# Optimization experiments

Measured on AMD Instinct MI355X. Metric: run time of the kernel, lower is better.

Reference implementation:

```python
import jax, jax.numpy as jnp
import numpy as np
import math

E_IN, E_OUT = 512, 96
B, QL, PL = 64, 128, 196

def _lin(k, shape):
    fan_in = shape[1]
    bound = 1.0 / math.sqrt(fan_in)
    k1, k2 = jax.random.split(k)
    W = jax.random.uniform(k1, shape, jnp.float32, -bound, bound)
    b = jax.random.uniform(k2, (shape[0],), jnp.float32, -bound, bound)
    return W, b

def setup_inputs() -> dict:
    key = jax.random.key(0)
    ks = jax.random.split(key, 16)
    inp = {
        'z_d_cls': jax.random.normal(ks[0], (B, E_IN), jnp.float32),
        'Z_d_tok': jax.random.normal(ks[1], (B, QL, E_IN), jnp.float32),
        'z_t_cls': jax.random.normal(ks[2], (B, E_IN), jnp.float32),
        'Z_t_tok': jax.random.normal(ks[3], (B, QL, E_IN), jnp.float32),
        'z_v_cls': jax.random.normal(ks[4], (B, E_IN), jnp.float32),
        'Z_v_patch': jax.random.normal(ks[5], (B, PL, E_IN), jnp.float32),
    }
    names = ['t_cls', 'd_cls', 'v_cls', 't_tok', 'v_patch', 'tgl_q', 'tgl_k', 'tgl_v']
    for i, n in enumerate(names):
        W, b = _lin(ks[6 + i], (E_OUT, E_IN))
        inp[f'W_{n}'] = W
        inp[f'b_{n}'] = b
    inp['ln_g'] = jnp.ones((E_OUT,), jnp.float32)
    inp['ln_b'] = jnp.zeros((E_OUT,), jnp.float32)
    return inp

def _l2n(x, eps=1e-6):
    return x / jnp.maximum(jnp.linalg.norm(x, axis=-1, keepdims=True), eps)

def _proj(x, W, b):
    return x @ W.T + b

def _layer_norm(x, g, b, eps=1e-5):
    mu = jnp.mean(x, axis=-1, keepdims=True)
    var = jnp.mean((x - mu) ** 2, axis=-1, keepdims=True)
    return (x - mu) / jnp.sqrt(var + eps) * g + b

def reference(z_d_cls, Z_d_tok, z_t_cls, Z_t_tok, z_v_cls, Z_v_patch,
              W_t_cls, b_t_cls, W_d_cls, b_d_cls, W_v_cls, b_v_cls,
              W_t_tok, b_t_tok, W_v_patch, b_v_patch,
              W_tgl_q, b_tgl_q, W_tgl_k, b_tgl_k, W_tgl_v, b_tgl_v,
              ln_g, ln_b):
    # --- TGG: global-global text/doc cosine sim [B, B]
    t = _l2n(_proj(z_t_cls, W_t_cls, b_t_cls))
    d = _l2n(_proj(z_d_cls, W_d_cls, b_d_cls))
    S_TGG = t @ d.T
    # --- TGL: cross-attention over all batch pairs
    Q = _proj(Z_d_tok, W_tgl_q, b_tgl_q)   # [b, q, h]
    K = _proj(Z_t_tok, W_tgl_k, b_tgl_k)   # [c, k, h]
    V = _proj(Z_t_tok, W_tgl_v, b_tgl_v)   # [c, k, h]
    scores = jnp.einsum('bqh,ckh->bcqk', Q, K) / math.sqrt(E_OUT)
    attn = jax.nn.softmax(scores, axis=-1)
    context = jnp.einsum('bcqk,ckh->bcqh', attn, V).mean(axis=2)  # [b, c, h]
    context = _layer_norm(context, ln_g, ln_b)
    S_TGL = jnp.einsum('ih,ijh->ij', d, _l2n(context))
    S_TIB = 0.5 * (S_TGG + S_TGL)
    # --- CGG: global-global text/vision cosine sim
    v = _l2n(_proj(z_v_cls, W_v_cls, b_v_cls))
    S_CGG = t @ v.T
    # --- CLL: token-patch max similarity
    t_tok = _l2n(_proj(Z_t_tok, W_t_tok, b_t_tok))        # [b, t, h]
    v_pat = _l2n(_proj(Z_v_patch, W_v_patch, b_v_patch))  # [c, p, h]
    sim = jnp.einsum('bth,cph->bctp', t_tok, v_pat)
    S_CLL = sim.max(axis=(-1, -2))
    S_CAB = 0.5 * (S_CGG + S_CLL)
    return S_TIB + S_CAB
```

## Files before the change

### kernel.cpp

```cpp
#include <hip/hip_runtime.h>
#include <hip/hip_bf16.h>
#include <math.h>

typedef __bf16 bf16;
typedef __attribute__((ext_vector_type(8))) __bf16 bf16x8;
typedef __attribute__((ext_vector_type(2))) float f32x2;
typedef __attribute__((ext_vector_type(4))) float f32x4;
typedef __attribute__((ext_vector_type(4))) unsigned int uint4v;

#define MFMA16(a, b, c) __builtin_amdgcn_mfma_f32_16x16x32_bf16(a, b, c, 0, 0, 0)

#define QSCALE 0.14724450f

__device__ __forceinline__ bf16x8 cvt8v(f32x4 lo, f32x4 hi) {
    bf16x8 r;
    r[0] = (bf16)lo[0]; r[1] = (bf16)lo[1]; r[2] = (bf16)lo[2]; r[3] = (bf16)lo[3];
    r[4] = (bf16)hi[0]; r[5] = (bf16)hi[1]; r[6] = (bf16)hi[2]; r[7] = (bf16)hi[3];
    return r;
}


struct WPtrs { const float* W[8]; };

__global__ __launch_bounds__(256) void cvtw_kernel(WPtrs wp, bf16* __restrict__ Wb) {
    int j   = blockIdx.x / 48;
    int blk = blockIdx.x - j * 48;
    int idx = (blk * 256 + threadIdx.x) * 4;
    f32x4 v = *(const f32x4*)(wp.W[j] + idx);
    bf16* dst = Wb + j * 49152 + idx;
    dst[0] = (bf16)v[0]; dst[1] = (bf16)v[1]; dst[2] = (bf16)v[2]; dst[3] = (bf16)v[3];
}


struct ProjParams {
    const float* src[8];
    const float* B[8];
    void* dst[8];
    const bf16* Wb;
};

__global__ __launch_bounds__(256) void proj_kernel(ProjParams p) {
    int w = threadIdx.x >> 6, lane = threadIdx.x & 63;
    int gw = blockIdx.x * 4 + w;
    int m = lane & 15, quad = lane >> 4;

    int job, t0;
    if      (gw < 256)  { job = 3; t0 = gw; }
    else if (gw < 512)  { job = 4; t0 = gw - 256; }
    else if (gw < 768)  { job = 5; t0 = gw - 512; }
    else if (gw < 1024) { job = 6; t0 = gw - 768; }
    else if (gw < 1416) { job = 7; t0 = gw - 1024; }
    else if (gw < 1422) { int r = gw - 1416; job = r >> 1; t0 = r & 1; }
    else return;
    int r0 = t0 << 5;

    const float* X = p.src[job] + (size_t)(r0 + m) * 512 + quad * 8;
    const bf16*  W = p.Wb + job * 49152 + (size_t)m * 512 + quad * 8;

    f32x4 acc[2][6] = {};
    #pragma unroll
    for (int kk = 0; kk < 512; kk += 32) {
        bf16x8 a0 = cvt8v(*(const f32x4*)(X + kk),
                          *(const f32x4*)(X + kk + 4));
        bf16x8 a1 = cvt8v(*(const f32x4*)(X + 16 * 512 + kk),
                          *(const f32x4*)(X + 16 * 512 + kk + 4));
        #pragma unroll
        for (int nt = 0; nt < 6; nt++) {
            bf16x8 b = *(const bf16x8*)(W + (size_t)nt * 16 * 512 + kk);
            acc[0][nt] = MFMA16(a0, b, acc[0][nt]);
            acc[1][nt] = MFMA16(a1, b, acc[1][nt]);
        }
    }

    bool  norm  = (job < 3) || (job >= 6);
    float scale = (job == 3) ? QSCALE : 1.0f;
    const float* Bv = p.B[job];
    float bb[6];
    #pragma unroll
    for (int nt = 0; nt < 6; nt++) bb[nt] = Bv[nt * 16 + m];

    #pragma unroll
    for (int rt = 0; rt < 2; rt++)
        #pragma unroll
        for (int nt = 0; nt < 6; nt++)
            #pragma unroll
            for (int r = 0; r < 4; r++)
                acc[rt][nt][r] = (acc[rt][nt][r] + bb[nt]) * scale;

    if (norm) {
        #pragma unroll
        for (int rt = 0; rt < 2; rt++)
            #pragma unroll
            for (int r = 0; r < 4; r++) {
                float s = 0.0f;
                #pragma unroll
                for (int nt = 0; nt < 6; nt++) s += acc[rt][nt][r] * acc[rt][nt][r];
                s += __shfl_xor(s, 1); s += __shfl_xor(s, 2);
                s += __shfl_xor(s, 4); s += __shfl_xor(s, 8);
                float inv = 1.0f / fmaxf(sqrtf(s), 1e-6f);
                #pragma unroll
                for (int nt = 0; nt < 6; nt++) acc[rt][nt][r] *= inv;
            }
    }

    if (job < 3) {
        float* dst = (float*)p.dst[job];
        #pragma unroll
        for (int rt = 0; rt < 2; rt++)
            #pragma unroll
            for (int r = 0; r < 4; r++)
                #pragma unroll
                for (int nt = 0; nt < 6; nt++)
                    dst[(size_t)(r0 + rt * 16 + quad * 4 + r) * 96 + nt * 16 + m] = acc[rt][nt][r];
    } else {
        bf16* dst = (bf16*)p.dst[job];
        #pragma unroll
        for (int rt = 0; rt < 2; rt++)
            #pragma unroll
            for (int r = 0; r < 4; r++)
                #pragma unroll
                for (int nt = 0; nt < 6; nt++)
                    dst[(size_t)(r0 + rt * 16 + quad * 4 + r) * 96 + nt * 16 + m] = (bf16)acc[rt][nt][r];
    }
}


__global__ __launch_bounds__(256) void attn_kernel(
    const bf16* __restrict__ Qg, const bf16* __restrict__ Kg, const bf16* __restrict__ Vg,
    float* __restrict__ Ctx)
{
    int pr = blockIdx.x;
    int b = pr >> 6, c = pr & 63;
    int tid = threadIdx.x, lane = tid & 63, w = tid >> 6;
    int m = lane & 15, quad = lane >> 4;
    const bf16* Q = Qg + (size_t)b * (128 * 96);
    const bf16* K = Kg + (size_t)c * (128 * 96);
    const bf16* V = Vg + (size_t)c * (128 * 96);

    __shared__ __align__(16) bf16 Klds[128 * 104];
    #pragma unroll
    for (int it = 0; it < 6; it++) {
        int ch = it * 256 + tid;
        int row = ch / 12, seg = ch - row * 12;
        *(uint4v*)(Klds + row * 104 + seg * 8) = *(const uint4v*)(K + ch * 8);
    }
    __syncthreads();

    f32x4 acc[2][8] = {};
    #pragma unroll
    for (int kk = 0; kk < 96; kk += 32) {
        bf16x8 a0 = *(const bf16x8*)(Q + (size_t)(w * 32 + m) * 96 + kk + quad * 8);
        bf16x8 a1 = *(const bf16x8*)(Q + (size_t)(w * 32 + 16 + m) * 96 + kk + quad * 8);
        #pragma unroll
        for (int nt = 0; nt < 8; nt++) {
            bf16x8 bb = *(const bf16x8*)(Klds + (nt * 16 + m) * 104 + kk + quad * 8);
            acc[0][nt] = MFMA16(a0, bb, acc[0][nt]);
            acc[1][nt] = MFMA16(a1, bb, acc[1][nt]);
        }
    }
    float wpart[8];
    #pragma unroll
    for (int nt = 0; nt < 8; nt++) wpart[nt] = 0.0f;
    #pragma unroll
    for (int mt = 0; mt < 2; mt++) {
        #pragma unroll
        for (int r = 0; r < 4; r++) {
            float tv[8]; float s = 0.0f;
            #pragma unroll
            for (int nt = 0; nt < 8; nt++) { tv[nt] = exp2f(acc[mt][nt][r]); s += tv[nt]; }
            s += __shfl_xor(s, 1); s += __shfl_xor(s, 2);
            s += __shfl_xor(s, 4); s += __shfl_xor(s, 8);
            float inv = 1.0f / s;
            #pragma unroll
            for (int nt = 0; nt < 8; nt++) wpart[nt] += tv[nt] * inv;
        }
    }
    #pragma unroll
    for (int nt = 0; nt < 8; nt++) {
        wpart[nt] += __shfl_xor(wpart[nt], 16);
        wpart[nt] += __shfl_xor(wpart[nt], 32);
    }
    __shared__ float wsum4[4][128];
    __shared__ float wk[128];
    __shared__ float ctxp[4][96];
    if (lane < 16) {
        #pragma unroll
        for (int nt = 0; nt < 8; nt++) wsum4[w][nt * 16 + lane] = wpart[nt];
    }
    __syncthreads();
    if (tid < 128) wk[tid] = wsum4[0][tid] + wsum4[1][tid] + wsum4[2][tid] + wsum4[3][tid];
    __syncthreads();
    {
        float c0 = 0.0f, c1 = 0.0f;
        if (lane < 48) {
            #pragma unroll 4
            for (int r = 0; r < 32; r++) {
                int k = w * 32 + r;
                unsigned u = *(const unsigned*)(V + (size_t)k * 96 + lane * 2);
                float lo = __uint_as_float(u << 16);
                float hi = __uint_as_float(u & 0xffff0000u);
                float wkk = wk[k];
                c0 += wkk * lo; c1 += wkk * hi;
            }
            ctxp[w][lane * 2]     = c0;
            ctxp[w][lane * 2 + 1] = c1;
        }
    }
    __syncthreads();
    if (tid < 96)
        Ctx[(size_t)pr * 96 + tid] =
            (ctxp[0][tid] + ctxp[1][tid] + ctxp[2][tid] + ctxp[3][tid]) * (1.0f / 128.0f);
}


__global__ __launch_bounds__(256) void cll_kernel(
    const bf16* __restrict__ Tt, const bf16* __restrict__ Vp,
    const float* __restrict__ Ctx, const float* __restrict__ t,
    const float* __restrict__ d, const float* __restrict__ v,
    const float* __restrict__ ln_g, const float* __restrict__ ln_b,
    float* __restrict__ out)
{
    int c = blockIdx.x >> 3, bg = blockIdx.x & 7;
    int tid = threadIdx.x, lane = tid & 63, w = tid >> 6;
    int m = lane & 15, quad = lane >> 4;
    const bf16* P = Vp + (size_t)c * (196 * 96);

    __shared__ __align__(16) bf16 Plds[196 * 104];
    __shared__ float red[8][4];
    for (int ch = tid; ch < 2352; ch += 256) {
        int row = ch / 12, seg = ch - row * 12;
        *(uint4v*)(Plds + row * 104 + seg * 8) = *(const uint4v*)(P + ch * 8);
    }
    int rofs[13];
    #pragma unroll
    for (int nt = 0; nt < 13; nt++) {
        int r = nt * 16 + m; if (r > 195) r = 195;
        rofs[nt] = r * 104;
    }
    __syncthreads();

    for (int bi = 0; bi < 8; bi++) {
        const bf16* T = Tt + (size_t)(bg * 8 + bi) * (128 * 96);
        f32x4 acc[2][13] = {};
        #pragma unroll
        for (int kk = 0; kk < 96; kk += 32) {
            bf16x8 a0 = *(const bf16x8*)(T + (size_t)(w * 32 + m) * 96 + kk + quad * 8);
            bf16x8 a1 = *(const bf16x8*)(T + (size_t)(w * 32 + 16 + m) * 96 + kk + quad * 8);
            #pragma unroll
            for (int nt = 0; nt < 13; nt++) {
                bf16x8 bb = *(const bf16x8*)(Plds + rofs[nt] + kk + quad * 8);
                acc[0][nt] = MFMA16(a0, bb, acc[0][nt]);
                acc[1][nt] = MFMA16(a1, bb, acc[1][nt]);
            }
        }
        float mx = -3.4e38f;
        #pragma unroll
        for (int mt = 0; mt < 2; mt++)
            #pragma unroll
            for (int nt = 0; nt < 13; nt++)
                #pragma unroll
                for (int r = 0; r < 4; r++) mx = fmaxf(mx, acc[mt][nt][r]);
        #pragma unroll
        for (int dd = 1; dd < 64; dd <<= 1) mx = fmaxf(mx, __shfl_xor(mx, dd));
        if (lane == 0) red[bi][w] = mx;
    }
    __syncthreads();

    #pragma unroll
    for (int half = 0; half < 2; half++) {
        int bi = w + half * 4;
        int i  = bg * 8 + bi;
        int pr = i * 64 + c;
        float scll = fmaxf(fmaxf(red[bi][0], red[bi][1]), fmaxf(red[bi][2], red[bi][3]));
        bool act = lane < 48;
        float c0 = 0, c1 = 0, t0 = 0, t1 = 0;
        float dj0 = 0, dj1 = 0, di0 = 0, di1 = 0, v0 = 0, v1 = 0, g0 = 0, g1 = 0, bb0 = 0, bb1 = 0;
        if (act) {
            f32x2 cc  = *(const f32x2*)(Ctx + (size_t)pr * 96 + lane * 2);
            f32x2 tt  = *(const f32x2*)(t + i * 96 + lane * 2);
            f32x2 ddj = *(const f32x2*)(d + c * 96 + lane * 2);
            f32x2 ddi = *(const f32x2*)(d + i * 96 + lane * 2);
            f32x2 vv  = *(const f32x2*)(v + c * 96 + lane * 2);
            f32x2 gg  = *(const f32x2*)(ln_g + lane * 2);
            f32x2 bbv = *(const f32x2*)(ln_b + lane * 2);
            c0 = cc[0]; c1 = cc[1]; t0 = tt[0]; t1 = tt[1];
            dj0 = ddj[0]; dj1 = ddj[1]; di0 = ddi[0]; di1 = ddi[1];
            v0 = vv[0]; v1 = vv[1];
            g0 = gg[0]; g1 = gg[1]; bb0 = bbv[0]; bb1 = bbv[1];
        }
        float s = c0 + c1;
        #pragma unroll
        for (int k = 1; k < 64; k <<= 1) s += __shfl_xor(s, k);
        float mean = s * (1.0f / 96.0f);
        float e0 = act ? (c0 - mean) : 0.0f;
        float e1 = act ? (c1 - mean) : 0.0f;
        float q = e0 * e0 + e1 * e1;
        #pragma unroll
        for (int k = 1; k < 64; k <<= 1) q += __shfl_xor(q, k);
        float rstd = rsqrtf(q * (1.0f / 96.0f) + 1e-5f);
        float y0 = act ? (e0 * rstd * g0 + bb0) : 0.0f;
        float y1 = act ? (e1 * rstd * g1 + bb1) : 0.0f;
        float dot = y0 * di0 + y1 * di1;
        float ssq = y0 * y0 + y1 * y1;
        float tg  = t0 * dj0 + t1 * dj1;
        float cg  = t0 * v0 + t1 * v1;
        #pragma unroll
        for (int k = 1; k < 64; k <<= 1) {
            dot += __shfl_xor(dot, k); ssq += __shfl_xor(ssq, k);
            tg  += __shfl_xor(tg, k);  cg  += __shfl_xor(cg, k);
        }
        if (lane == 0) {
            float stgl = dot / fmaxf(sqrtf(ssq), 1e-6f);
            out[pr] = 0.5f * (tg + stgl) + 0.5f * (cg + scll);
        }
    }
}


extern "C" void kernel_launch(void* const* d_in, const int* in_sizes, int n_in,
                              void* d_out, int out_size, void* d_ws, size_t ws_size,
                              hipStream_t stream)
{
    (void)in_sizes; (void)n_in; (void)out_size; (void)ws_size;
    char* ws = (char*)d_ws;
    float* t     = (float*)(ws + 0);
    float* d     = (float*)(ws + 24576);
    float* v     = (float*)(ws + 49152);
    bf16* Wb = (bf16*)(ws + 106496);
    bf16* Qb = (bf16*)(ws + 892928);
    bf16* Kb = (bf16*)(ws + 892928 + 1572864);
    bf16* Vb = (bf16*)(ws + 892928 + 2 * 1572864);
    bf16* Tt = (bf16*)(ws + 892928 + 3 * 1572864);
    bf16* Vp = (bf16*)(ws + 892928 + 4 * 1572864);
    float* Ctx = (float*)(ws + 892928 + 4 * 1572864 + 2408448);

    WPtrs wp;
    wp.W[0] = (const float*)d_in[6];
    wp.W[1] = (const float*)d_in[8];
    wp.W[2] = (const float*)d_in[10];
    wp.W[3] = (const float*)d_in[16];
    wp.W[4] = (const float*)d_in[18];
    wp.W[5] = (const float*)d_in[20];
    wp.W[6] = (const float*)d_in[12];
    wp.W[7] = (const float*)d_in[14];
    hipLaunchKernelGGL(cvtw_kernel, dim3(384), dim3(256), 0, stream, wp, Wb);

    ProjParams pp;
    pp.Wb = Wb;
    pp.src[0] = (const float*)d_in[2];  pp.B[0] = (const float*)d_in[7];  pp.dst[0] = t;
    pp.src[1] = (const float*)d_in[0];  pp.B[1] = (const float*)d_in[9];  pp.dst[1] = d;
    pp.src[2] = (const float*)d_in[4];  pp.B[2] = (const float*)d_in[11]; pp.dst[2] = v;
    pp.src[3] = (const float*)d_in[1];  pp.B[3] = (const float*)d_in[17]; pp.dst[3] = Qb;
    pp.src[4] = (const float*)d_in[3];  pp.B[4] = (const float*)d_in[19]; pp.dst[4] = Kb;
    pp.src[5] = (const float*)d_in[3];  pp.B[5] = (const float*)d_in[21]; pp.dst[5] = Vb;
    pp.src[6] = (const float*)d_in[3];  pp.B[6] = (const float*)d_in[13]; pp.dst[6] = Tt;
    pp.src[7] = (const float*)d_in[5];  pp.B[7] = (const float*)d_in[15]; pp.dst[7] = Vp;
    hipLaunchKernelGGL(proj_kernel, dim3(356), dim3(256), 0, stream, pp);

    hipLaunchKernelGGL(attn_kernel, dim3(4096), dim3(256), 0, stream,
                       (const bf16*)Qb, (const bf16*)Kb, (const bf16*)Vb, Ctx);
    hipLaunchKernelGGL(cll_kernel, dim3(512), dim3(256), 0, stream,
                       (const bf16*)Tt, (const bf16*)Vp,
                       (const float*)Ctx, (const float*)t, (const float*)d, (const float*)v,
                       (const float*)d_in[22], (const float*)d_in[23], (float*)d_out);
}
```

Before: 240.7 us.

## Drop weight-conversion kernel, XOR-swizzle LDS tiles, prefetch V into registers

```diff
diff --git a/kernel.cpp b/kernel.cpp
--- a/kernel.cpp
+++ b/kernel.cpp
@@ -20,23 +20,11 @@
 }
 
 
-struct WPtrs { const float* W[8]; };
-
-__global__ __launch_bounds__(256) void cvtw_kernel(WPtrs wp, bf16* __restrict__ Wb) {
-    int j   = blockIdx.x / 48;
-    int blk = blockIdx.x - j * 48;
-    int idx = (blk * 256 + threadIdx.x) * 4;
-    f32x4 v = *(const f32x4*)(wp.W[j] + idx);
-    bf16* dst = Wb + j * 49152 + idx;
-    dst[0] = (bf16)v[0]; dst[1] = (bf16)v[1]; dst[2] = (bf16)v[2]; dst[3] = (bf16)v[3];
-}
-
-
 struct ProjParams {
     const float* src[8];
+    const float* W[8];
     const float* B[8];
     void* dst[8];
-    const bf16* Wb;
 };
 
 __global__ __launch_bounds__(256) void proj_kernel(ProjParams p) {
@@ -54,8 +42,8 @@
     else return;
     int r0 = t0 << 5;
 
-    const float* X = p.src[job] + (size_t)(r0 + m) * 512 + quad * 8;
-    const bf16*  W = p.Wb + job * 49152 + (size_t)m * 512 + quad * 8;
+    const float* X  = p.src[job] + (size_t)(r0 + m) * 512 + quad * 8;
+    const float* Wf = p.W[job] + (size_t)m * 512 + quad * 8;
 
     f32x4 acc[2][6] = {};
     #pragma unroll
@@ -66,7 +54,8 @@
                           *(const f32x4*)(X + 16 * 512 + kk + 4));
         #pragma unroll
         for (int nt = 0; nt < 6; nt++) {
-            bf16x8 b = *(const bf16x8*)(W + (size_t)nt * 16 * 512 + kk);
+            const float* wp = Wf + (size_t)nt * 16 * 512 + kk;
+            bf16x8 b = cvt8v(*(const f32x4*)wp, *(const f32x4*)(wp + 4));
             acc[0][nt] = MFMA16(a0, b, acc[0][nt]);
             acc[1][nt] = MFMA16(a1, b, acc[1][nt]);
         }
@@ -137,15 +126,18 @@
     const bf16* K = Kg + (size_t)c * (128 * 96);
     const bf16* V = Vg + (size_t)c * (128 * 96);
 
-    __shared__ __align__(16) bf16 Klds[128 * 104];
+    __shared__ __align__(16) bf16 Klds[128 * 96];
+    char* kb = (char*)Klds;
     #pragma unroll
     for (int it = 0; it < 6; it++) {
         int ch = it * 256 + tid;
         int row = ch / 12, seg = ch - row * 12;
-        *(uint4v*)(Klds + row * 104 + seg * 8) = *(const uint4v*)(K + ch * 8);
-    }
-    __syncthreads();
-
+        int addr = (row * 192 + seg * 16) ^ ((row & 7) << 4);
+        *(uint4v*)(kb + addr) = *(const uint4v*)(K + ch * 8);
+    }
+    __syncthreads();
+
+    int kx = (m & 7) << 4;
     f32x4 acc[2][8] = {};
     #pragma unroll
     for (int kk = 0; kk < 96; kk += 32) {
@@ -153,11 +145,20 @@
         bf16x8 a1 = *(const bf16x8*)(Q + (size_t)(w * 32 + 16 + m) * 96 + kk + quad * 8);
         #pragma unroll
         for (int nt = 0; nt < 8; nt++) {
-            bf16x8 bb = *(const bf16x8*)(Klds + (nt * 16 + m) * 104 + kk + quad * 8);
+            int addr = ((nt * 16 + m) * 192 + kk * 2 + quad * 16) ^ kx;
+            bf16x8 bb = *(const bf16x8*)(kb + addr);
             acc[0][nt] = MFMA16(a0, bb, acc[0][nt]);
             acc[1][nt] = MFMA16(a1, bb, acc[1][nt]);
         }
     }
+
+    unsigned vr[32];
+    if (lane < 48) {
+        #pragma unroll
+        for (int r = 0; r < 32; r++)
+            vr[r] = *(const unsigned*)(V + (size_t)(w * 32 + r) * 96 + lane * 2);
+    }
+
     float wpart[8];
     #pragma unroll
     for (int nt = 0; nt < 8; nt++) wpart[nt] = 0.0f;
@@ -170,7 +171,7 @@
             for (int nt = 0; nt < 8; nt++) { tv[nt] = exp2f(acc[mt][nt][r]); s += tv[nt]; }
             s += __shfl_xor(s, 1); s += __shfl_xor(s, 2);
             s += __shfl_xor(s, 4); s += __shfl_xor(s, 8);
-            float inv = 1.0f / s;
+            float inv = __builtin_amdgcn_rcpf(s);
             #pragma unroll
             for (int nt = 0; nt < 8; nt++) wpart[nt] += tv[nt] * inv;
         }
@@ -193,14 +194,12 @@
     {
         float c0 = 0.0f, c1 = 0.0f;
         if (lane < 48) {
-            #pragma unroll 4
+            #pragma unroll
             for (int r = 0; r < 32; r++) {
-                int k = w * 32 + r;
-                unsigned u = *(const unsigned*)(V + (size_t)k * 96 + lane * 2);
-                float lo = __uint_as_float(u << 16);
-                float hi = __uint_as_float(u & 0xffff0000u);
-                float wkk = wk[k];
-                c0 += wkk * lo; c1 += wkk * hi;
+                unsigned u = vr[r];
+                float wkk = wk[w * 32 + r];
+                c0 += wkk * __uint_as_float(u << 16);
+                c1 += wkk * __uint_as_float(u & 0xffff0000u);
             }
             ctxp[w][lane * 2]     = c0;
             ctxp[w][lane * 2 + 1] = c1;
@@ -225,17 +224,20 @@
     int m = lane & 15, quad = lane >> 4;
     const bf16* P = Vp + (size_t)c * (196 * 96);
 
-    __shared__ __align__(16) bf16 Plds[196 * 104];
+    __shared__ __align__(16) bf16 Plds[196 * 96];
     __shared__ float red[8][4];
+    char* pb = (char*)Plds;
     for (int ch = tid; ch < 2352; ch += 256) {
         int row = ch / 12, seg = ch - row * 12;
-        *(uint4v*)(Plds + row * 104 + seg * 8) = *(const uint4v*)(P + ch * 8);
-    }
-    int rofs[13];
+        int addr = (row * 192 + seg * 16) ^ ((row & 7) << 4);
+        *(uint4v*)(pb + addr) = *(const uint4v*)(P + ch * 8);
+    }
+    int rofs[13], rx[13];
     #pragma unroll
     for (int nt = 0; nt < 13; nt++) {
         int r = nt * 16 + m; if (r > 195) r = 195;
-        rofs[nt] = r * 104;
+        rofs[nt] = r * 192 + quad * 16;
+        rx[nt]   = (r & 7) << 4;
     }
     __syncthreads();
 
@@ -248,7 +250,7 @@
             bf16x8 a1 = *(const bf16x8*)(T + (size_t)(w * 32 + 16 + m) * 96 + kk + quad * 8);
             #pragma unroll
             for (int nt = 0; nt < 13; nt++) {
-                bf16x8 bb = *(const bf16x8*)(Plds + rofs[nt] + kk + quad * 8);
+                bf16x8 bb = *(const bf16x8*)(pb + ((rofs[nt] + kk * 2) ^ rx[nt]));
                 acc[0][nt] = MFMA16(a0, bb, acc[0][nt]);
                 acc[1][nt] = MFMA16(a1, bb, acc[1][nt]);
             }
@@ -326,7 +328,6 @@
     float* t     = (float*)(ws + 0);
     float* d     = (float*)(ws + 24576);
     float* v     = (float*)(ws + 49152);
-    bf16* Wb = (bf16*)(ws + 106496);
     bf16* Qb = (bf16*)(ws + 892928);
     bf16* Kb = (bf16*)(ws + 892928 + 1572864);
     bf16* Vb = (bf16*)(ws + 892928 + 2 * 1572864);
@@ -334,27 +335,15 @@
     bf16* Vp = (bf16*)(ws + 892928 + 4 * 1572864);
     float* Ctx = (float*)(ws + 892928 + 4 * 1572864 + 2408448);
 
-    WPtrs wp;
-    wp.W[0] = (const float*)d_in[6];
-    wp.W[1] = (const float*)d_in[8];
-    wp.W[2] = (const float*)d_in[10];
-    wp.W[3] = (const float*)d_in[16];
-    wp.W[4] = (const float*)d_in[18];
-    wp.W[5] = (const float*)d_in[20];
-    wp.W[6] = (const float*)d_in[12];
-    wp.W[7] = (const float*)d_in[14];
-    hipLaunchKernelGGL(cvtw_kernel, dim3(384), dim3(256), 0, stream, wp, Wb);
-
     ProjParams pp;
-    pp.Wb = Wb;
-    pp.src[0] = (const float*)d_in[2];  pp.B[0] = (const float*)d_in[7];  pp.dst[0] = t;
-    pp.src[1] = (const float*)d_in[0];  pp.B[1] = (const float*)d_in[9];  pp.dst[1] = d;
-    pp.src[2] = (const float*)d_in[4];  pp.B[2] = (const float*)d_in[11]; pp.dst[2] = v;
-    pp.src[3] = (const float*)d_in[1];  pp.B[3] = (const float*)d_in[17]; pp.dst[3] = Qb;
-    pp.src[4] = (const float*)d_in[3];  pp.B[4] = (const float*)d_in[19]; pp.dst[4] = Kb;
-    pp.src[5] = (const float*)d_in[3];  pp.B[5] = (const float*)d_in[21]; pp.dst[5] = Vb;
-    pp.src[6] = (const float*)d_in[3];  pp.B[6] = (const float*)d_in[13]; pp.dst[6] = Tt;
-    pp.src[7] = (const float*)d_in[5];  pp.B[7] = (const float*)d_in[15]; pp.dst[7] = Vp;
+    pp.src[0] = (const float*)d_in[2];  pp.W[0] = (const float*)d_in[6];  pp.B[0] = (const float*)d_in[7];  pp.dst[0] = t;
+    pp.src[1] = (const float*)d_in[0];  pp.W[1] = (const float*)d_in[8];  pp.B[1] = (const float*)d_in[9];  pp.dst[1] = d;
+    pp.src[2] = (const float*)d_in[4];  pp.W[2] = (const float*)d_in[10]; pp.B[2] = (const float*)d_in[11]; pp.dst[2] = v;
+    pp.src[3] = (const float*)d_in[1];  pp.W[3] = (const float*)d_in[16]; pp.B[3] = (const float*)d_in[17]; pp.dst[3] = Qb;
+    pp.src[4] = (const float*)d_in[3];  pp.W[4] = (const float*)d_in[18]; pp.B[4] = (const float*)d_in[19]; pp.dst[4] = Kb;
+    pp.src[5] = (const float*)d_in[3];  pp.W[5] = (const float*)d_in[20]; pp.B[5] = (const float*)d_in[21]; pp.dst[5] = Vb;
+    pp.src[6] = (const float*)d_in[3];  pp.W[6] = (const float*)d_in[12]; pp.B[6] = (const float*)d_in[13]; pp.dst[6] = Tt;
+    pp.src[7] = (const float*)d_in[5];  pp.W[7] = (const float*)d_in[14]; pp.B[7] = (const float*)d_in[15]; pp.dst[7] = Vp;
     hipLaunchKernelGGL(proj_kernel, dim3(356), dim3(256), 0, stream, pp);
 
     hipLaunchKernelGGL(attn_kernel, dim3(4096), dim3(256), 0, stream,
```

Measured after the change: 264.5 us. 9.9% more time.

## Fuse K/V/T projections sharing input, swizzle LDS, prefetch V in attention

Applied to the files above, without the earlier changes.

```diff
diff --git a/kernel.cpp b/kernel.cpp
--- a/kernel.cpp
+++ b/kernel.cpp
@@ -44,83 +44,112 @@
     int gw = blockIdx.x * 4 + w;
     int m = lane & 15, quad = lane >> 4;
 
-    int job, t0;
-    if      (gw < 256)  { job = 3; t0 = gw; }
-    else if (gw < 512)  { job = 4; t0 = gw - 256; }
-    else if (gw < 768)  { job = 5; t0 = gw - 512; }
-    else if (gw < 1024) { job = 6; t0 = gw - 768; }
-    else if (gw < 1416) { job = 7; t0 = gw - 1024; }
-    else if (gw < 1422) { int r = gw - 1416; job = r >> 1; t0 = r & 1; }
-    else return;
-    int r0 = t0 << 5;
-
-    const float* X = p.src[job] + (size_t)(r0 + m) * 512 + quad * 8;
-    const bf16*  W = p.Wb + job * 49152 + (size_t)m * 512 + quad * 8;
-
-    f32x4 acc[2][6] = {};
-    #pragma unroll
-    for (int kk = 0; kk < 512; kk += 32) {
-        bf16x8 a0 = cvt8v(*(const f32x4*)(X + kk),
-                          *(const f32x4*)(X + kk + 4));
-        bf16x8 a1 = cvt8v(*(const f32x4*)(X + 16 * 512 + kk),
-                          *(const f32x4*)(X + 16 * 512 + kk + 4));
-        #pragma unroll
-        for (int nt = 0; nt < 6; nt++) {
-            bf16x8 b = *(const bf16x8*)(W + (size_t)nt * 16 * 512 + kk);
-            acc[0][nt] = MFMA16(a0, b, acc[0][nt]);
-            acc[1][nt] = MFMA16(a1, b, acc[1][nt]);
-        }
-    }
-
-    bool  norm  = (job < 3) || (job >= 6);
-    float scale = (job == 3) ? QSCALE : 1.0f;
-    const float* Bv = p.B[job];
-    float bb[6];
-    #pragma unroll
-    for (int nt = 0; nt < 6; nt++) bb[nt] = Bv[nt * 16 + m];
-
-    #pragma unroll
-    for (int rt = 0; rt < 2; rt++)
-        #pragma unroll
-        for (int nt = 0; nt < 6; nt++)
-            #pragma unroll
-            for (int r = 0; r < 4; r++)
-                acc[rt][nt][r] = (acc[rt][nt][r] + bb[nt]) * scale;
-
-    if (norm) {
-        #pragma unroll
-        for (int rt = 0; rt < 2; rt++)
-            #pragma unroll
-            for (int r = 0; r < 4; r++) {
-                float s = 0.0f;
+    if (gw >= 512 && gw < 1024) {
+        int r0 = (gw - 512) << 4;
+        const float* X  = p.src[4] + (size_t)(r0 + m) * 512 + quad * 8;
+        const bf16*  W4 = p.Wb + 4 * 49152 + (size_t)m * 512 + quad * 8;
+
+        f32x4 acc[3][6] = {};
+        #pragma unroll
+        for (int kk = 0; kk < 512; kk += 32) {
+            bf16x8 a = cvt8v(*(const f32x4*)(X + kk), *(const f32x4*)(X + kk + 4));
+            #pragma unroll
+            for (int j = 0; j < 3; j++)
                 #pragma unroll
-                for (int nt = 0; nt < 6; nt++) s += acc[rt][nt][r] * acc[rt][nt][r];
-                s += __shfl_xor(s, 1); s += __shfl_xor(s, 2);
-                s += __shfl_xor(s, 4); s += __shfl_xor(s, 8);
-                float inv = 1.0f / fmaxf(sqrtf(s), 1e-6f);
+                for (int nt = 0; nt < 6; nt++) {
+                    bf16x8 b = *(const bf16x8*)(W4 + j * 49152 + (size_t)nt * 16 * 512 + kk);
+                    acc[j][nt] = MFMA16(a, b, acc[j][nt]);
+                }
+        }
+        #pragma unroll
+        for (int j = 0; j < 3; j++) {
+            const float* Bv = p.B[4 + j];
+            #pragma unroll
+            for (int nt = 0; nt < 6; nt++) {
+                float bv = Bv[nt * 16 + m];
                 #pragma unroll
-                for (int nt = 0; nt < 6; nt++) acc[rt][nt][r] *= inv;
+                for (int r = 0; r < 4; r++) acc[j][nt][r] += bv;
             }
-    }
-
-    if (job < 3) {
-        float* dst = (float*)p.dst[job];
-        #pragma unroll
-        for (int rt = 0; rt < 2; rt++)
+            if (j == 2) {
+                #pragma unroll
+                for (int r = 0; r < 4; r++) {
+                    float s = 0.0f;
+                    #pragma unroll
+                    for (int nt = 0; nt < 6; nt++) s += acc[2][nt][r] * acc[2][nt][r];
+                    s += __shfl_xor(s, 1); s += __shfl_xor(s, 2);
+                    s += __shfl_xor(s, 4); s += __shfl_xor(s, 8);
+                    float inv = 1.0f / fmaxf(sqrtf(s), 1e-6f);
+                    #pragma unroll
+                    for (int nt = 0; nt < 6; nt++) acc[2][nt][r] *= inv;
+                }
+            }
+            bf16* dst = (bf16*)p.dst[4 + j];
             #pragma unroll
             for (int r = 0; r < 4; r++)
                 #pragma unroll
                 for (int nt = 0; nt < 6; nt++)
-                    dst[(size_t)(r0 + rt * 16 + quad * 4 + r) * 96 + nt * 16 + m] = acc[rt][nt][r];
+                    dst[(size_t)(r0 + quad * 4 + r) * 96 + nt * 16 + m] = (bf16)acc[j][nt][r];
+        }
+        return;
+    }
+
+    int job, t0;
+    if      (gw < 512)  { job = 3; t0 = gw; }
+    else if (gw < 1808) { job = 7; t0 = gw - 1024; }
+    else if (gw < 1820) { int r = gw - 1808; job = r >> 2; t0 = r & 3; }
+    else return;
+    int r0 = t0 << 4;
+
+    const float* X = p.src[job] + (size_t)(r0 + m) * 512 + quad * 8;
+    const bf16*  W = p.Wb + job * 49152 + (size_t)m * 512 + quad * 8;
+
+    f32x4 acc[6] = {};
+    #pragma unroll
+    for (int kk = 0; kk < 512; kk += 32) {
+        bf16x8 a = cvt8v(*(const f32x4*)(X + kk), *(const f32x4*)(X + kk + 4));
+        #pragma unroll
+        for (int nt = 0; nt < 6; nt++) {
+            bf16x8 b = *(const bf16x8*)(W + (size_t)nt * 16 * 512 + kk);
+            acc[nt] = MFMA16(a, b, acc[nt]);
+        }
+    }
+
+    bool  norm  = (job != 3);
+    float scale = (job == 3) ? QSCALE : 1.0f;
+    const float* Bv = p.B[job];
+    #pragma unroll
+    for (int nt = 0; nt < 6; nt++) {
+        float bv = Bv[nt * 16 + m];
+        #pragma unroll
+        for (int r = 0; r < 4; r++) acc[nt][r] = (acc[nt][r] + bv) * scale;
+    }
+    if (norm) {
+        #pragma unroll
+        for (int r = 0; r < 4; r++) {
+            float s = 0.0f;
+            #pragma unroll
+            for (int nt = 0; nt < 6; nt++) s += acc[nt][r] * acc[nt][r];
+            s += __shfl_xor(s, 1); s += __shfl_xor(s, 2);
+            s += __shfl_xor(s, 4); s += __shfl_xor(s, 8);
+            float inv = 1.0f / fmaxf(sqrtf(s), 1e-6f);
+            #pragma unroll
+            for (int nt = 0; nt < 6; nt++) acc[nt][r] *= inv;
+        }
+    }
+    if (job < 3) {
+        float* dst = (float*)p.dst[job];
+        #pragma unroll
+        for (int r = 0; r < 4; r++)
+            #pragma unroll
+            for (int nt = 0; nt < 6; nt++)
+                dst[(size_t)(r0 + quad * 4 + r) * 96 + nt * 16 + m] = acc[nt][r];
     } else {
         bf16* dst = (bf16*)p.dst[job];
         #pragma unroll
-        for (int rt = 0; rt < 2; rt++)
-            #pragma unroll
-            for (int r = 0; r < 4; r++)
-                #pragma unroll
-                for (int nt = 0; nt < 6; nt++)
-                    dst[(size_t)(r0 + rt * 16 + quad * 4 + r) * 96 + nt * 16 + m] = (bf16)acc[rt][nt][r];
+        for (int r = 0; r < 4; r++)
+            #pragma unroll
+            for (int nt = 0; nt < 6; nt++)
+                dst[(size_t)(r0 + quad * 4 + r) * 96 + nt * 16 + m] = (bf16)acc[nt][r];
     }
 }
 
@@ -137,15 +166,18 @@
     const bf16* K = Kg + (size_t)c * (128 * 96);
     const bf16* V = Vg + (size_t)c * (128 * 96);
 
-    __shared__ __align__(16) bf16 Klds[128 * 104];
+    __shared__ __align__(16) bf16 Klds[128 * 96];
+    char* kb = (char*)Klds;
     #pragma unroll
     for (int it = 0; it < 6; it++) {
         int ch = it * 256 + tid;
         int row = ch / 12, seg = ch - row * 12;
-        *(uint4v*)(Klds + row * 104 + seg * 8) = *(const uint4v*)(K + ch * 8);
-    }
-    __syncthreads();
-
+        int addr = (row * 192 + seg * 16) ^ ((row & 7) << 4);
+        *(uint4v*)(kb + addr) = *(const uint4v*)(K + ch * 8);
+    }
+    __syncthreads();
+
+    int kx = (m & 7) << 4;
     f32x4 acc[2][8] = {};
     #pragma unroll
     for (int kk = 0; kk < 96; kk += 32) {
@@ -153,11 +185,20 @@
         bf16x8 a1 = *(const bf16x8*)(Q + (size_t)(w * 32 + 16 + m) * 96 + kk + quad * 8);
         #pragma unroll
         for (int nt = 0; nt < 8; nt++) {
-            bf16x8 bb = *(const bf16x8*)(Klds + (nt * 16 + m) * 104 + kk + quad * 8);
+            int addr = ((nt * 16 + m) * 192 + kk * 2 + quad * 16) ^ kx;
+            bf16x8 bb = *(const bf16x8*)(kb + addr);
             acc[0][nt] = MFMA16(a0, bb, acc[0][nt]);
             acc[1][nt] = MFMA16(a1, bb, acc[1][nt]);
         }
     }
+
+    unsigned vr[32];
+    if (lane < 48) {
+        #pragma unroll
+        for (int r = 0; r < 32; r++)
+            vr[r] = *(const unsigned*)(V + (size_t)(w * 32 + r) * 96 + lane * 2);
+    }
+
     float wpart[8];
     #pragma unroll
     for (int nt = 0; nt < 8; nt++) wpart[nt] = 0.0f;
@@ -170,7 +211,7 @@
             for (int nt = 0; nt < 8; nt++) { tv[nt] = exp2f(acc[mt][nt][r]); s += tv[nt]; }
             s += __shfl_xor(s, 1); s += __shfl_xor(s, 2);
             s += __shfl_xor(s, 4); s += __shfl_xor(s, 8);
-            float inv = 1.0f / s;
+            float inv = __builtin_amdgcn_rcpf(s);
             #pragma unroll
             for (int nt = 0; nt < 8; nt++) wpart[nt] += tv[nt] * inv;
         }
@@ -193,14 +234,12 @@
     {
         float c0 = 0.0f, c1 = 0.0f;
         if (lane < 48) {
-            #pragma unroll 4
+            #pragma unroll
             for (int r = 0; r < 32; r++) {
-                int k = w * 32 + r;
-                unsigned u = *(const unsigned*)(V + (size_t)k * 96 + lane * 2);
-                float lo = __uint_as_float(u << 16);
-                float hi = __uint_as_float(u & 0xffff0000u);
-                float wkk = wk[k];
-                c0 += wkk * lo; c1 += wkk * hi;
+                unsigned u = vr[r];
+                float wkk = wk[w * 32 + r];
+                c0 += wkk * __uint_as_float(u << 16);
+                c1 += wkk * __uint_as_float(u & 0xffff0000u);
             }
             ctxp[w][lane * 2]     = c0;
             ctxp[w][lane * 2 + 1] = c1;
@@ -225,17 +264,20 @@
     int m = lane & 15, quad = lane >> 4;
     const bf16* P = Vp + (size_t)c * (196 * 96);
 
-    __shared__ __align__(16) bf16 Plds[196 * 104];
+    __shared__ __align__(16) bf16 Plds[196 * 96];
     __shared__ float red[8][4];
+    char* pb = (char*)Plds;
     for (int ch = tid; ch < 2352; ch += 256) {
         int row = ch / 12, seg = ch - row * 12;
-        *(uint4v*)(Plds + row * 104 + seg * 8) = *(const uint4v*)(P + ch * 8);
-    }
-    int rofs[13];
+        int addr = (row * 192 + seg * 16) ^ ((row & 7) << 4);
+        *(uint4v*)(pb + addr) = *(const uint4v*)(P + ch * 8);
+    }
+    int rofs[13], rx[13];
     #pragma unroll
     for (int nt = 0; nt < 13; nt++) {
         int r = nt * 16 + m; if (r > 195) r = 195;
-        rofs[nt] = r * 104;
+        rofs[nt] = r * 192 + quad * 16;
+        rx[nt]   = (r & 7) << 4;
     }
     __syncthreads();
 
@@ -248,7 +290,7 @@
             bf16x8 a1 = *(const bf16x8*)(T + (size_t)(w * 32 + 16 + m) * 96 + kk + quad * 8);
             #pragma unroll
             for (int nt = 0; nt < 13; nt++) {
-                bf16x8 bb = *(const bf16x8*)(Plds + rofs[nt] + kk + quad * 8);
+                bf16x8 bb = *(const bf16x8*)(pb + ((rofs[nt] + kk * 2) ^ rx[nt]));
                 acc[0][nt] = MFMA16(a0, bb, acc[0][nt]);
                 acc[1][nt] = MFMA16(a1, bb, acc[1][nt]);
             }
@@ -355,7 +397,7 @@
     pp.src[5] = (const float*)d_in[3];  pp.B[5] = (const float*)d_in[21]; pp.dst[5] = Vb;
     pp.src[6] = (const float*)d_in[3];  pp.B[6] = (const float*)d_in[13]; pp.dst[6] = Tt;
     pp.src[7] = (const float*)d_in[5];  pp.B[7] = (const float*)d_in[15]; pp.dst[7] = Vp;
-    hipLaunchKernelGGL(proj_kernel, dim3(356), dim3(256), 0, stream, pp);
+    hipLaunchKernelGGL(proj_kernel, dim3(455), dim3(256), 0, stream, pp);
 
     hipLaunchKernelGGL(attn_kernel, dim3(4096), dim3(256), 0, stream,
                        (const bf16*)Qb, (const bf16*)Kb, (const bf16*)Vb, Ctx);
```

After: 272.3 us. 1.13x slower.
